# Kernel tuning notes

Measured on AMD Instinct MI355X. Metric: run time of the kernel, lower is better.

## Reference

```python
import jax, jax.numpy as jnp
import numpy as np

N_NODES = 100000
N_EDGES = 500000
N_REL = 4
N_LAYERS = 4
IN_FEAT = 64
EMB = 128
N_GRAPHS = 64


def setup_inputs() -> dict:
    key = jax.random.key(0)
    ks = jax.random.split(key, 16)
    x = jax.random.normal(ks[0], (N_NODES, IN_FEAT), dtype=jnp.float32)
    eis = [jax.random.randint(ks[1 + r], (2, N_EDGES), 0, N_NODES, dtype=jnp.int32) for r in range(N_REL)]
    batch = jnp.sort(jax.random.randint(ks[5], (N_NODES,), 0, N_GRAPHS, dtype=jnp.int32))
    s = 1.0 / np.sqrt(IN_FEAT)
    emb_w = jax.random.uniform(ks[6], (IN_FEAT, EMB), jnp.float32, -s, s)
    emb_b = jax.random.uniform(ks[7], (EMB,), jnp.float32, -s, s)
    t = 1.0 / np.sqrt(EMB)
    root_w = jax.random.uniform(ks[8], (N_LAYERS, EMB, EMB), jnp.float32, -t, t)
    root_b = jax.random.uniform(ks[9], (N_LAYERS, EMB), jnp.float32, -t, t)
    conv_w = jax.random.uniform(ks[10], (N_LAYERS, N_REL, EMB, EMB), jnp.float32, -t, t)
    return {"x": x, "edge_index0": eis[0], "edge_index1": eis[1], "edge_index2": eis[2],
            "edge_index3": eis[3], "batch": batch, "emb_w": emb_w, "emb_b": emb_b,
            "root_w": root_w, "root_b": root_b, "conv_w": conv_w}


def _scatter_max(msgs, dst, num_nodes):
    # PyG max aggregation: unmatched nodes get 0
    agg = jax.ops.segment_max(msgs, dst, num_segments=num_nodes)
    return jnp.where(jnp.isfinite(agg), agg, 0.0)


def reference(x, edge_index0, edge_index1, edge_index2, edge_index3, batch,
              emb_w, emb_b, root_w, root_b, conv_w):
    edges = [edge_index0, edge_index1, edge_index2, edge_index3]
    h = x @ emb_w + emb_b  # [N, EMB]
    for l in range(N_LAYERS):
        out = h @ root_w[l] + root_b[l]
        for r in range(N_REL):
            src, dst = edges[r][0], edges[r][1]
            m = (h @ conv_w[l, r])[src]  # linear then gather: [E, EMB]
            out = out + _scatter_max(m, dst, N_NODES)
        h = jax.nn.relu(out)
    # global_add_pool
    return jax.ops.segment_sum(h, batch, num_segments=N_GRAPHS)
```

## Files before the change

kernel.cpp:

```cpp
#include <hip/hip_runtime.h>

#define NN 100000
#define NE 500000
#define NR 4
#define NL 4
#define FIN 64
#define D 128
#define NGR 64

#define FP 8
#define PSZ ((NN + FP - 1) / FP)
#define EPB 4096

typedef __attribute__((ext_vector_type(8))) short short8;
typedef __attribute__((ext_vector_type(4))) float f32x4;
typedef __attribute__((ext_vector_type(2))) unsigned short u16x2;
typedef unsigned short ushort;
typedef unsigned int uint;

__device__ __forceinline__ ushort f2b(float f) {
    uint u = __float_as_uint(f);
    uint r = (u + 0x7fffu + ((u >> 16) & 1u)) >> 16;
    return (ushort)r;
}
__device__ __forceinline__ float b2f(ushort b) {
    return __uint_as_float(((uint)b) << 16);
}
__device__ __forceinline__ ushort enc16(ushort u) {
    return u ^ (ushort)((((short)u) >> 15) | (short)0x8000);
}
__device__ __forceinline__ ushort dec16(ushort k) {
    return k ^ (ushort)((((short)(k ^ 0x8000)) >> 15) | (short)0x8000);
}
__device__ __forceinline__ u16x2 vmax2(u16x2 a, u16x2 b) {
#if __has_builtin(__builtin_elementwise_max)
    return __builtin_elementwise_max(a, b);
#else
    u16x2 r;
    r.x = a.x > b.x ? a.x : b.x;
    r.y = a.y > b.y ? a.y : b.y;
    return r;
#endif
}

__global__ void zero_i32(int* __restrict__ p, int n) {
    int i = blockIdx.x * blockDim.x + threadIdx.x;
    if (i < n) p[i] = 0;
}
__global__ void zero_f32(float* __restrict__ p, int n) {
    int i = blockIdx.x * blockDim.x + threadIdx.x;
    if (i < n) p[i] = 0.f;
}
__global__ void xcvt(const float* __restrict__ x, ushort* __restrict__ xb, int n) {
    int i = blockIdx.x * blockDim.x + threadIdx.x;
    if (i < n) xb[i] = f2b(x[i]);
}

__global__ void wperm_kernel(const float* __restrict__ W, ushort* __restrict__ dst,
                             int K, int total) {
    int i = blockIdx.x * blockDim.x + threadIdx.x;
    if (i >= total) return;
    int per = K * 128;
    int mi = i / per;
    int o = i - mi * per;
    int j = o & 7, lane = (o >> 3) & 63, rest = o >> 9;
    int K032 = K / 32;
    int k0 = rest % K032, t = rest / K032;
    int k = k0 * 32 + (lane >> 4) * 8 + j;
    int n = t * 16 + (lane & 15);
    dst[i] = f2b(W[(size_t)mi * per + k * 128 + n]);
}

template <int CAP>
__global__ __launch_bounds__(256) void slot_fill(const int* __restrict__ e0,
                                                 const int* __restrict__ e1,
                                                 const int* __restrict__ e2,
                                                 const int* __restrict__ e3,
                                                 int* __restrict__ deg,
                                                 int* __restrict__ slots) {
    const int part = blockIdx.x % FP;
    const int chunk = blockIdx.x / FP;
    const int plo = part * PSZ;
    const int phi = (plo + PSZ < NN) ? plo + PSZ : NN;
    const int i0 = chunk * EPB;
    int i1 = i0 + EPB; if (i1 > NR * NE) i1 = NR * NE;
    for (int i = i0 + threadIdx.x; i < i1; i += 256) {
        int r = i / NE, j = i - r * NE;
        const int* ei = (r == 0) ? e0 : (r == 1) ? e1 : (r == 2) ? e2 : e3;
        int d = ei[NE + j];
        if (d >= plo && d < phi) {
            int s = ei[j];
            int slot = atomicAdd(&deg[r * NN + d], 1);
            if (slot < CAP)
                slots[((size_t)r * NN + d) * CAP + slot] = s * (D * 2);
        }
    }
}

template <int K, int MODE>
__global__ __launch_bounds__(256) void mgemm(const ushort* __restrict__ A,
                                             const ushort* __restrict__ Bp,
                                             const float* __restrict__ bias,
                                             ushort* __restrict__ Ch) {
    constexpr int K032 = K / 32;
    __shared__ ushort Bs[8 * K032 * 64 * 8];
    const int tid = threadIdx.x;
    for (int i = tid; i < K * 16; i += 256)
        ((float4*)Bs)[i] = ((const float4*)Bp)[i];
    const int lane = tid & 63, wave = tid >> 6;
    const int quad = lane >> 4, l15 = lane & 15;
    const int ch = wave & 1, rg = wave >> 1;
    __syncthreads();
    short8 breg[4][K032];
#pragma unroll
    for (int tt = 0; tt < 4; tt++)
#pragma unroll
        for (int k0 = 0; k0 < K032; k0++)
            breg[tt][k0] = *(const short8*)&Bs[(size_t)(((ch * 4 + tt) * K032 + k0) * 64 + lane) * 8];
    float bv[4] = {0.f, 0.f, 0.f, 0.f};
    if (bias)
#pragma unroll
        for (int tt = 0; tt < 4; tt++) bv[tt] = bias[(ch * 4 + tt) * 16 + l15];
    for (int tile = blockIdx.x; tile < NN / 32; tile += gridDim.x) {
        const int row0 = tile * 32 + rg * 16;
        const ushort* Ar = A + (size_t)(row0 + l15) * K + quad * 8;
        short8 a[K032];
#pragma unroll
        for (int k0 = 0; k0 < K032; k0++) a[k0] = *(const short8*)(Ar + k0 * 32);
        f32x4 acc[4];
#pragma unroll
        for (int tt = 0; tt < 4; tt++) acc[tt] = (f32x4){bv[tt], bv[tt], bv[tt], bv[tt]};
#pragma unroll
        for (int k0 = 0; k0 < K032; k0++)
#pragma unroll
            for (int tt = 0; tt < 4; tt++)
                acc[tt] = __builtin_amdgcn_mfma_f32_16x16x32_bf16(a[k0], breg[tt][k0], acc[tt], 0, 0, 0);
#pragma unroll
        for (int tt = 0; tt < 4; tt++) {
            const int col = (ch * 4 + tt) * 16 + l15;
#pragma unroll
            for (int r = 0; r < 4; r++) {
                ushort v = f2b(acc[tt][r]);
                if (MODE == 1) v = enc16(v);
                Ch[(size_t)(row0 + quad * 4 + r) * D + col] = v;
            }
        }
    }
}

__global__ __launch_bounds__(256) void mgemm5(const ushort* __restrict__ A,
                                              const ushort* __restrict__ wpRootL,
                                              const ushort* __restrict__ wpConvL,
                                              const float* __restrict__ biasL,
                                              ushort* __restrict__ ob,
                                              ushort* __restrict__ mbuf) {
    constexpr int K032 = 4;
    const int m = blockIdx.y;
    const ushort* Bp = (m == 0) ? wpRootL : wpConvL + (size_t)(m - 1) * 128 * 128;
    ushort* Ch = (m == 0) ? ob : mbuf + (size_t)(m - 1) * NN * D;
    const bool key = (m != 0);
    __shared__ ushort Bs[8 * K032 * 64 * 8];
    const int tid = threadIdx.x;
    for (int i = tid; i < 128 * 16; i += 256)
        ((float4*)Bs)[i] = ((const float4*)Bp)[i];
    const int lane = tid & 63, wave = tid >> 6;
    const int quad = lane >> 4, l15 = lane & 15;
    const int ch = wave & 1, rg = wave >> 1;
    __syncthreads();
    short8 breg[4][K032];
#pragma unroll
    for (int tt = 0; tt < 4; tt++)
#pragma unroll
        for (int k0 = 0; k0 < K032; k0++)
            breg[tt][k0] = *(const short8*)&Bs[(size_t)(((ch * 4 + tt) * K032 + k0) * 64 + lane) * 8];
    float bv[4] = {0.f, 0.f, 0.f, 0.f};
    if (m == 0)
#pragma unroll
        for (int tt = 0; tt < 4; tt++) bv[tt] = biasL[(ch * 4 + tt) * 16 + l15];
    for (int tile = blockIdx.x; tile < NN / 32; tile += gridDim.x) {
        const int row0 = tile * 32 + rg * 16;
        const ushort* Ar = A + (size_t)(row0 + l15) * 128 + quad * 8;
        short8 a[K032];
#pragma unroll
        for (int k0 = 0; k0 < K032; k0++) a[k0] = *(const short8*)(Ar + k0 * 32);
        f32x4 acc[4];
#pragma unroll
        for (int tt = 0; tt < 4; tt++) acc[tt] = (f32x4){bv[tt], bv[tt], bv[tt], bv[tt]};
#pragma unroll
        for (int k0 = 0; k0 < K032; k0++)
#pragma unroll
            for (int tt = 0; tt < 4; tt++)
                acc[tt] = __builtin_amdgcn_mfma_f32_16x16x32_bf16(a[k0], breg[tt][k0], acc[tt], 0, 0, 0);
#pragma unroll
        for (int tt = 0; tt < 4; tt++) {
            const int col = (ch * 4 + tt) * 16 + l15;
#pragma unroll
            for (int r = 0; r < 4; r++) {
                ushort v = f2b(acc[tt][r]);
                if (key) v = enc16(v);
                Ch[(size_t)(row0 + quad * 4 + r) * D + col] = v;
            }
        }
    }
}

template <int CAP>
__global__ __launch_bounds__(256) void agg_kernel(const ushort* __restrict__ mb,
                                                  const int* __restrict__ deg,
                                                  const int* __restrict__ slots,
                                                  int G,
                                                  const ushort* __restrict__ base,
                                                  ushort* __restrict__ outh,
                                                  int do_relu) {
    int wv = threadIdx.x >> 6;
    int lane = threadIdx.x & 63;
    int node = blockIdx.x * 4 + wv;
    if (node >= NN) return;
    uint bp = ((const uint*)(base + (size_t)node * D))[lane];
    float rx = __uint_as_float(bp << 16), ry = __uint_as_float(bp & 0xffff0000u);
    for (int g = 0; g < G; g++) {
        const char* ml = (const char*)(mb + (size_t)g * NN * D) + lane * 4;
        const int* sl = slots + ((size_t)g * NN + node) * CAP;
        int nd = deg[(size_t)g * NN + node];
        if (nd > CAP) nd = CAP;
        if (nd <= 0) continue;
        u16x2 a0 = (u16x2)0, a1 = (u16x2)0, a2 = (u16x2)0, a3 = (u16x2)0;
        int s_l = (lane < nd) ? sl[lane] : 0;
        int i = 0;
        for (; i + 4 <= nd; i += 4) {
            int s0 = __shfl(s_l, i + 0);
            int s1 = __shfl(s_l, i + 1);
            int s2 = __shfl(s_l, i + 2);
            int s3 = __shfl(s_l, i + 3);
            u16x2 v0 = *(const u16x2*)(ml + s0);
            u16x2 v1 = *(const u16x2*)(ml + s1);
            u16x2 v2 = *(const u16x2*)(ml + s2);
            u16x2 v3 = *(const u16x2*)(ml + s3);
            a0 = vmax2(a0, v0);
            a1 = vmax2(a1, v1);
            a2 = vmax2(a2, v2);
            a3 = vmax2(a3, v3);
        }
        for (; i < nd; i++) {
            int s = __shfl(s_l, i);
            a0 = vmax2(a0, *(const u16x2*)(ml + s));
        }
        u16x2 am = vmax2(vmax2(a0, a1), vmax2(a2, a3));
        rx += b2f(dec16(am.x));
        ry += b2f(dec16(am.y));
    }
    if (do_relu) { rx = fmaxf(rx, 0.f); ry = fmaxf(ry, 0.f); }
    uint pk = (uint)f2b(rx) | ((uint)f2b(ry) << 16);
    ((uint*)(outh + (size_t)node * D))[lane] = pk;
}

#define PCH 256
__global__ __launch_bounds__(128) void pool_kernel(const ushort* __restrict__ h,
                                                   const int* __restrict__ batch,
                                                   float* __restrict__ out) {
    int c = threadIdx.x;
    int n0 = blockIdx.x * PCH;
    if (n0 >= NN) return;
    int n1 = n0 + PCH; if (n1 > NN) n1 = NN;
    int cur = batch[n0];
    float acc = 0.f;
    for (int n = n0; n < n1; n++) {
        int g = batch[n];
        if (g != cur) {
            atomicAdd(&out[cur * D + c], acc);
            acc = 0.f;
            cur = g;
        }
        acc += b2f(h[(size_t)n * D + c]);
    }
    atomicAdd(&out[cur * D + c], acc);
}

extern "C" void kernel_launch(void* const* d_in, const int* in_sizes, int n_in,
                              void* d_out, int out_size, void* d_ws, size_t ws_size,
                              hipStream_t stream) {
    const float* x = (const float*)d_in[0];
    const int* ei[4] = {(const int*)d_in[1], (const int*)d_in[2],
                        (const int*)d_in[3], (const int*)d_in[4]};
    const int* batch = (const int*)d_in[5];
    const float* emb_w = (const float*)d_in[6];
    const float* emb_b = (const float*)d_in[7];
    const float* root_w = (const float*)d_in[8];
    const float* root_b = (const float*)d_in[9];
    const float* conv_w = (const float*)d_in[10];
    float* out = (float*)d_out;

    const size_t WPT = (size_t)FIN * 128 + 20 * (size_t)128 * 128;
    int G = 1, CAP = 32;
    {
        struct Cfg { int g, cap; } cfgs[] = {{4, 64}, {4, 32}, {2, 32}, {1, 32}};
        for (auto c : cfgs) {
            size_t need = ((size_t)NN * D * (2 + c.g) + (size_t)NN * FIN + WPT) * 2 +
                          ((size_t)NR * NN * (1 + c.cap)) * 4;
            if (ws_size >= need) { G = c.g; CAP = c.cap; break; }
        }
    }

    ushort* hb = (ushort*)d_ws;
    ushort* ob = hb + (size_t)NN * D;
    ushort* mbuf = ob + (size_t)NN * D;
    ushort* xb = mbuf + (size_t)G * NN * D;
    ushort* wp = xb + (size_t)NN * FIN;
    int* deg = (int*)(wp + WPT);
    int* slots = deg + (size_t)NR * NN;
    ushort* wpEmb = wp;
    ushort* wpRoot = wp + (size_t)FIN * 128;
    ushort* wpConv = wpRoot + (size_t)4 * 128 * 128;

    zero_i32<<<(NR * NN + 255) / 256, 256, 0, stream>>>(deg, NR * NN);
    {
        int nch = (NR * NE + EPB - 1) / EPB;
        if (CAP == 64)
            slot_fill<64><<<nch * FP, 256, 0, stream>>>(ei[0], ei[1], ei[2], ei[3], deg, slots);
        else
            slot_fill<32><<<nch * FP, 256, 0, stream>>>(ei[0], ei[1], ei[2], ei[3], deg, slots);
    }

    {
        int t1 = FIN * 128;
        wperm_kernel<<<(t1 + 255) / 256, 256, 0, stream>>>(emb_w, wpEmb, FIN, t1);
        int t2 = 4 * 128 * 128;
        wperm_kernel<<<(t2 + 255) / 256, 256, 0, stream>>>(root_w, wpRoot, 128, t2);
        int t3 = 16 * 128 * 128;
        wperm_kernel<<<(t3 + 255) / 256, 256, 0, stream>>>(conv_w, wpConv, 128, t3);
        int t4 = NN * FIN;
        xcvt<<<(t4 + 255) / 256, 256, 0, stream>>>(x, xb, t4);
    }

    mgemm<FIN, 0><<<1024, 256, 0, stream>>>(xb, wpEmb, emb_b, hb);

    for (int l = 0; l < NL; l++) {
        if (G == 4) {
            mgemm5<<<dim3(640, 5), 256, 0, stream>>>(hb, wpRoot + (size_t)l * 128 * 128,
                                                     wpConv + (size_t)l * 4 * 128 * 128,
                                                     root_b + (size_t)l * D, ob, mbuf);
            if (CAP == 64)
                agg_kernel<64><<<(NN + 3) / 4, 256, 0, stream>>>(mbuf, deg, slots, 4, ob, hb, 1);
            else
                agg_kernel<32><<<(NN + 3) / 4, 256, 0, stream>>>(mbuf, deg, slots, 4, ob, hb, 1);
        } else {
            mgemm<128, 0><<<1024, 256, 0, stream>>>(hb, wpRoot + (size_t)l * 128 * 128,
                                                    root_b + (size_t)l * D, ob);
            for (int g0 = 0; g0 < NR; g0 += G) {
                for (int r = g0; r < g0 + G; r++)
                    mgemm<128, 1><<<1024, 256, 0, stream>>>(
                        hb, wpConv + (size_t)(l * NR + r) * 128 * 128, nullptr,
                        mbuf + (size_t)(r - g0) * NN * D);
                int last = (g0 + G == NR);
                agg_kernel<32><<<(NN + 3) / 4, 256, 0, stream>>>(
                    mbuf, deg + (size_t)g0 * NN, slots + (size_t)g0 * NN * 32, G,
                    ob, last ? hb : ob, last ? 1 : 0);
            }
        }
    }

    zero_f32<<<(NGR * D + 255) / 256, 256, 0, stream>>>(out, NGR * D);
    pool_kernel<<<(NN + PCH - 1) / PCH, 128, 0, stream>>>(hb, batch, out);
}
```

Baseline: 947.3 us.

## Interleave relation slots per node and aggregate all relations in one loop

```diff
diff --git a/kernel.cpp b/kernel.cpp
--- a/kernel.cpp
+++ b/kernel.cpp
@@ -11,6 +11,7 @@
 #define FP 8
 #define PSZ ((NN + FP - 1) / FP)
 #define EPB 4096
+#define CAPS 32
 
 typedef __attribute__((ext_vector_type(8))) short short8;
 typedef __attribute__((ext_vector_type(4))) float f32x4;
@@ -54,6 +55,11 @@
 __global__ void xcvt(const float* __restrict__ x, ushort* __restrict__ xb, int n) {
     int i = blockIdx.x * blockDim.x + threadIdx.x;
     if (i < n) xb[i] = f2b(x[i]);
+}
+__global__ void zero_dummy(ushort* __restrict__ mbuf, int G) {
+    int i = blockIdx.x * blockDim.x + threadIdx.x;
+    if (i < G * D)
+        mbuf[(size_t)(i / D) * (NN + 1) * D + (size_t)NN * D + (i % D)] = 0;
 }
 
 __global__ void wperm_kernel(const float* __restrict__ W, ushort* __restrict__ dst,
@@ -71,7 +77,6 @@
     dst[i] = f2b(W[(size_t)mi * per + k * 128 + n]);
 }
 
-template <int CAP>
 __global__ __launch_bounds__(256) void slot_fill(const int* __restrict__ e0,
                                                  const int* __restrict__ e1,
                                                  const int* __restrict__ e2,
@@ -90,9 +95,9 @@
         int d = ei[NE + j];
         if (d >= plo && d < phi) {
             int s = ei[j];
-            int slot = atomicAdd(&deg[r * NN + d], 1);
-            if (slot < CAP)
-                slots[((size_t)r * NN + d) * CAP + slot] = s * (D * 2);
+            int slot = atomicAdd(&deg[d * NR + r], 1);
+            if (slot < CAPS)
+                slots[((size_t)d * NR + r) * CAPS + slot] = s * (D * 2);
         }
     }
 }
@@ -157,7 +162,7 @@
     constexpr int K032 = 4;
     const int m = blockIdx.y;
     const ushort* Bp = (m == 0) ? wpRootL : wpConvL + (size_t)(m - 1) * 128 * 128;
-    ushort* Ch = (m == 0) ? ob : mbuf + (size_t)(m - 1) * NN * D;
+    ushort* Ch = (m == 0) ? ob : mbuf + (size_t)(m - 1) * (NN + 1) * D;
     const bool key = (m != 0);
     __shared__ ushort Bs[8 * K032 * 64 * 8];
     const int tid = threadIdx.x;
@@ -204,50 +209,54 @@
     }
 }
 
-template <int CAP>
+template <int G>
 __global__ __launch_bounds__(256) void agg_kernel(const ushort* __restrict__ mb,
                                                   const int* __restrict__ deg,
                                                   const int* __restrict__ slots,
-                                                  int G,
+                                                  int g0,
                                                   const ushort* __restrict__ base,
                                                   ushort* __restrict__ outh,
                                                   int do_relu) {
-    int wv = threadIdx.x >> 6;
-    int lane = threadIdx.x & 63;
-    int node = blockIdx.x * 4 + wv;
+    const int wv = threadIdx.x >> 6;
+    const int lane = threadIdx.x & 63;
+    const int node = blockIdx.x * 4 + wv;
     if (node >= NN) return;
+    const int DUM = NN * D * 2;
+    const int* db = deg + (size_t)node * NR + g0;
+    const int* sb = slots + ((size_t)node * NR + g0) * CAPS;
+    int nd[G], s_l[G];
+    const char* ml[G];
+#pragma unroll
+    for (int g = 0; g < G; g++) {
+        int n = db[g];
+        nd[g] = (n > CAPS) ? CAPS : n;
+        s_l[g] = (lane < nd[g]) ? sb[g * CAPS + lane] : DUM;
+        ml[g] = (const char*)(mb + (size_t)g * (NN + 1) * D) + lane * 4;
+    }
+    int ndmax = 0;
+#pragma unroll
+    for (int g = 0; g < G; g++) ndmax = (nd[g] > ndmax) ? nd[g] : ndmax;
+    u16x2 acc[G];
+#pragma unroll
+    for (int g = 0; g < G; g++) acc[g] = (u16x2)0;
+    for (int i = 0; i < ndmax; i += 2) {
+#pragma unroll
+        for (int g = 0; g < G; g++) {
+            int sa = __shfl(s_l[g], i);
+            int sc = __shfl(s_l[g], i + 1);
+            sa = (i < nd[g]) ? sa : DUM;
+            sc = (i + 1 < nd[g]) ? sc : DUM;
+            u16x2 va = *(const u16x2*)(ml[g] + sa);
+            u16x2 vb = *(const u16x2*)(ml[g] + sc);
+            acc[g] = vmax2(acc[g], vmax2(va, vb));
+        }
+    }
     uint bp = ((const uint*)(base + (size_t)node * D))[lane];
     float rx = __uint_as_float(bp << 16), ry = __uint_as_float(bp & 0xffff0000u);
+#pragma unroll
     for (int g = 0; g < G; g++) {
-        const char* ml = (const char*)(mb + (size_t)g * NN * D) + lane * 4;
-        const int* sl = slots + ((size_t)g * NN + node) * CAP;
-        int nd = deg[(size_t)g * NN + node];
-        if (nd > CAP) nd = CAP;
-        if (nd <= 0) continue;
-        u16x2 a0 = (u16x2)0, a1 = (u16x2)0, a2 = (u16x2)0, a3 = (u16x2)0;
-        int s_l = (lane < nd) ? sl[lane] : 0;
-        int i = 0;
-        for (; i + 4 <= nd; i += 4) {
-            int s0 = __shfl(s_l, i + 0);
-            int s1 = __shfl(s_l, i + 1);
-            int s2 = __shfl(s_l, i + 2);
-            int s3 = __shfl(s_l, i + 3);
-            u16x2 v0 = *(const u16x2*)(ml + s0);
-            u16x2 v1 = *(const u16x2*)(ml + s1);
-            u16x2 v2 = *(const u16x2*)(ml + s2);
-            u16x2 v3 = *(const u16x2*)(ml + s3);
-            a0 = vmax2(a0, v0);
-            a1 = vmax2(a1, v1);
-            a2 = vmax2(a2, v2);
-            a3 = vmax2(a3, v3);
-        }
-        for (; i < nd; i++) {
-            int s = __shfl(s_l, i);
-            a0 = vmax2(a0, *(const u16x2*)(ml + s));
-        }
-        u16x2 am = vmax2(vmax2(a0, a1), vmax2(a2, a3));
-        rx += b2f(dec16(am.x));
-        ry += b2f(dec16(am.y));
+        rx += (nd[g] > 0) ? b2f(dec16(acc[g].x)) : 0.f;
+        ry += (nd[g] > 0) ? b2f(dec16(acc[g].y)) : 0.f;
     }
     if (do_relu) { rx = fmaxf(rx, 0.f); ry = fmaxf(ry, 0.f); }
     uint pk = (uint)f2b(rx) | ((uint)f2b(ry) << 16);
@@ -291,20 +300,17 @@
     float* out = (float*)d_out;
 
     const size_t WPT = (size_t)FIN * 128 + 20 * (size_t)128 * 128;
-    int G = 1, CAP = 32;
-    {
-        struct Cfg { int g, cap; } cfgs[] = {{4, 64}, {4, 32}, {2, 32}, {1, 32}};
-        for (auto c : cfgs) {
-            size_t need = ((size_t)NN * D * (2 + c.g) + (size_t)NN * FIN + WPT) * 2 +
-                          ((size_t)NR * NN * (1 + c.cap)) * 4;
-            if (ws_size >= need) { G = c.g; CAP = c.cap; break; }
-        }
+    int G = 1;
+    for (int g = 4; g >= 1; g >>= 1) {
+        size_t need = ((size_t)NN * D * 2 + (size_t)g * (NN + 1) * D + (size_t)NN * FIN + WPT) * 2 +
+                      ((size_t)NR * NN * (1 + CAPS)) * 4;
+        if (ws_size >= need) { G = g; break; }
     }
 
     ushort* hb = (ushort*)d_ws;
     ushort* ob = hb + (size_t)NN * D;
     ushort* mbuf = ob + (size_t)NN * D;
-    ushort* xb = mbuf + (size_t)G * NN * D;
+    ushort* xb = mbuf + (size_t)G * (NN + 1) * D;
     ushort* wp = xb + (size_t)NN * FIN;
     int* deg = (int*)(wp + WPT);
     int* slots = deg + (size_t)NR * NN;
@@ -315,10 +321,7 @@
     zero_i32<<<(NR * NN + 255) / 256, 256, 0, stream>>>(deg, NR * NN);
     {
         int nch = (NR * NE + EPB - 1) / EPB;
-        if (CAP == 64)
-            slot_fill<64><<<nch * FP, 256, 0, stream>>>(ei[0], ei[1], ei[2], ei[3], deg, slots);
-        else
-            slot_fill<32><<<nch * FP, 256, 0, stream>>>(ei[0], ei[1], ei[2], ei[3], deg, slots);
+        slot_fill<<<nch * FP, 256, 0, stream>>>(ei[0], ei[1], ei[2], ei[3], deg, slots);
     }
 
     {
@@ -330,6 +333,7 @@
         wperm_kernel<<<(t3 + 255) / 256, 256, 0, stream>>>(conv_w, wpConv, 128, t3);
         int t4 = NN * FIN;
         xcvt<<<(t4 + 255) / 256, 256, 0, stream>>>(x, xb, t4);
+        zero_dummy<<<(G * D + 255) / 256, 256, 0, stream>>>(mbuf, G);
     }
 
     mgemm<FIN, 0><<<1024, 256, 0, stream>>>(xb, wpEmb, emb_b, hb);
@@ -339,10 +343,7 @@
             mgemm5<<<dim3(640, 5), 256, 0, stream>>>(hb, wpRoot + (size_t)l * 128 * 128,
                                                      wpConv + (size_t)l * 4 * 128 * 128,
                                                      root_b + (size_t)l * D, ob, mbuf);
-            if (CAP == 64)
-                agg_kernel<64><<<(NN + 3) / 4, 256, 0, stream>>>(mbuf, deg, slots, 4, ob, hb, 1);
-            else
-                agg_kernel<32><<<(NN + 3) / 4, 256, 0, stream>>>(mbuf, deg, slots, 4, ob, hb, 1);
+            agg_kernel<4><<<(NN + 3) / 4, 256, 0, stream>>>(mbuf, deg, slots, 0, ob, hb, 1);
         } else {
             mgemm<128, 0><<<1024, 256, 0, stream>>>(hb, wpRoot + (size_t)l * 128 * 128,
                                                     root_b + (size_t)l * D, ob);
@@ -350,11 +351,14 @@
                 for (int r = g0; r < g0 + G; r++)
                     mgemm<128, 1><<<1024, 256, 0, stream>>>(
                         hb, wpConv + (size_t)(l * NR + r) * 128 * 128, nullptr,
-                        mbuf + (size_t)(r - g0) * NN * D);
+                        mbuf + (size_t)(r - g0) * (NN + 1) * D);
                 int last = (g0 + G == NR);
-                agg_kernel<32><<<(NN + 3) / 4, 256, 0, stream>>>(
-                    mbuf, deg + (size_t)g0 * NN, slots + (size_t)g0 * NN * 32, G,
-                    ob, last ? hb : ob, last ? 1 : 0);
+                if (G == 2)
+                    agg_kernel<2><<<(NN + 3) / 4, 256, 0, stream>>>(
+                        mbuf, deg, slots, g0, ob, last ? hb : ob, last ? 1 : 0);
+                else
+                    agg_kernel<1><<<(NN + 3) / 4, 256, 0, stream>>>(
+                        mbuf, deg, slots, g0, ob, last ? hb : ob, last ? 1 : 0);
             }
         }
     }
```

Result: faster. 860.4 us (-9.2%).
